# Kernel optimization log

Measured on AMD Instinct MI355X. Metric: run time of the kernel, lower is better.

## Reference

```python
import math
import jax, jax.numpy as jnp
import numpy as np

jax.config.update("jax_enable_x64", True)

P_PRIME = 1000003            # prime modulus; p-1 = 2*3*166667
N_FACTORS = (2, 3, 166667)   # prime factors of p-1 (for primitive-root search)
B, NPATCH, L, K, DIM = 4, 784, 9, 16, 28  # batch, patches/sample, patch len, kernels, map dim


def _modpow(base, exp, p, nbits=21):
    """Vectorized modular exponentiation (square-and-multiply), int64, exponents < 2^nbits."""
    shape = jnp.broadcast_shapes(jnp.shape(base), jnp.shape(exp))
    b0 = jnp.broadcast_to(jnp.asarray(base, jnp.int64) % p, shape)
    e = jnp.broadcast_to(jnp.asarray(exp, jnp.int64), shape)
    def body(i, c):
        res, b = c
        res = jnp.where(((e >> i) & 1) == 1, (res * b) % p, res)
        return (res, (b * b) % p)
    res, _ = jax.lax.fori_loop(0, nbits, body, (jnp.ones(shape, jnp.int64), b0))
    return res


def _decrypt_ips(ct0, cts, y, sk_y, g, p):
    """IPFE decrypt + BSGS discrete log. ct0:[B,P] cts:[B,P,L] y:[K,L] sk_y:[K] -> signed ip [K,B,P]."""
    n = p - 1
    powed = _modpow(cts[None], jnp.mod(y, n)[:, None, None, :], p)   # [K,B,P,L]
    num = powed[..., 0]
    for i in range(1, L):                                            # fixed small L=9
        num = (num * powed[..., i]) % p
    denom = _modpow(ct0[None], jnp.mod(sk_y, n)[:, None, None], p)   # [K,B,P]
    val = (num * _modpow(denom, p - 2, p)) % p                       # = g^{<x,y>} mod p (Fermat inverse)
    # baby-step giant-step over group order n
    m = math.isqrt(n - 1) + 1
    n_giant = -(-n // m)
    baby = _modpow(jnp.int64(g), jnp.arange(m, dtype=jnp.int64), p)  # g^j, j in [0,m)
    order = jnp.argsort(baby)
    sb = baby[order]
    ginv_m = _modpow(jnp.int64(g), jnp.int64((n - m) % n), p)        # g^{-m}
    pt = _modpow(ginv_m, jnp.arange(n_giant, dtype=jnp.int64), p)    # g^{-m*i}
    gamma = (val.reshape(-1)[:, None] * pt[None, :]) % p             # [T, n_giant] giant steps
    pos = jnp.clip(jnp.searchsorted(sb, gamma), 0, m - 1)
    hit = sb[pos] == gamma
    cand = jnp.arange(n_giant, dtype=jnp.int64)[None, :] * m + order[pos]
    ip = jnp.min(jnp.where(hit, cand, n), axis=1)                    # unique match: ip = i*m + j
    ip = jnp.where(ip > n // 2, ip - n, ip)                          # signed representative
    return ip.reshape(K, ct0.shape[0], ct0.shape[1])


def _bn(x, g_, b_, m_, v_):
    s = g_ * jax.lax.rsqrt(v_ + 1e-5)
    return (x - m_[None, :, None, None]) * s[None, :, None, None] + b_[None, :, None, None]


def _conv(x, w, b):
    o = jax.lax.conv_general_dilated(x, w, (1, 1), ((1, 1), (1, 1)),
                                     dimension_numbers=("NCHW", "OIHW", "NCHW"))
    return o + b[None, :, None, None]


def _pool(x):
    return jax.lax.reduce_window(x, jnp.array(-jnp.inf, x.dtype), jax.lax.max,
                                 (1, 1, 2, 2), (1, 1, 2, 2), "VALID")


def _forward(ct0, cts, y, sk_y, bias1, bn1_g, bn1_b, bn1_m, bn1_v,
             conv2_w, conv2_b, bn2_g, bn2_b, bn2_m, bn2_v,
             conv3_w, conv3_b, bn3_g, bn3_b, bn3_m, bn3_v,
             fc1_w, fc1_b, fc2_w, fc2_b, g, p):
    ip = _decrypt_ips(ct0, cts, y, sk_y, g, p)                       # [K,B,P] int64
    maps = ip.astype(jnp.float32) / 10000.0 + bias1[:, None, None]   # dequantize + conv1 bias
    feat = jnp.transpose(maps, (1, 0, 2)).reshape(-1, K, DIM, DIM)   # [B,16,28,28]
    feat = _pool(jax.nn.relu(_bn(feat, bn1_g, bn1_b, bn1_m, bn1_v)))
    feat = _pool(jax.nn.relu(_bn(_conv(feat, conv2_w, conv2_b), bn2_g, bn2_b, bn2_m, bn2_v)))
    feat = _pool(jax.nn.relu(_bn(_conv(feat, conv3_w, conv3_b), bn3_g, bn3_b, bn3_m, bn3_v)))
    flat = feat.reshape(feat.shape[0], -1)                           # [B,576]
    h = jax.nn.relu(flat @ fc1_w.T + fc1_b)                          # dropout = identity (eval mode)
    return h @ fc2_w.T + fc2_b                                       # [B,10]


def setup_inputs():
    rng = np.random.default_rng(0)
    p, n = P_PRIME, P_PRIME - 1
    assert all(p % d for d in range(2, math.isqrt(p) + 1))           # p prime
    g = next(gg for gg in range(2, 200)
             if all(pow(gg, n // q, p) != 1 for q in N_FACTORS))      # primitive root mod p
    s = rng.integers(1, n, size=L)                                    # master secret
    pk = [pow(g, int(si), p) for si in s]
    y = rng.integers(-50, 51, size=(K, L)).astype(np.int64)          # round(w*10000)
    x = rng.integers(0, 21, size=(B, NPATCH, L))                     # quantized patch values
    r = rng.integers(1, n, size=(B, NPATCH))
    gx = [pow(g, t, p) for t in range(21)]
    ct0 = np.zeros((B, NPATCH), dtype=np.int64)
    cts = np.zeros((B, NPATCH, L), dtype=np.int64)
    for b in range(B):
        for j in range(NPATCH):
            rr = int(r[b, j])
            ct0[b, j] = pow(g, rr, p)
            for i in range(L):
                cts[b, j, i] = pow(pk[i], rr, p) * gx[x[b, j, i]] % p
    sk_y = np.array([sum(int(s[i]) * int(y[k, i]) for i in range(L)) % n
                     for k in range(K)], dtype=np.int64)
    f32 = lambda a: jnp.asarray(a, jnp.float32)
    def rn(*sh):
        return f32(rng.standard_normal(sh) * 0.1)
    def bnp(c):
        return (f32(1.0 + 0.1 * rng.standard_normal(c)), rn(c), rn(c), f32(rng.random(c) + 0.5))
    bn1_g, bn1_b, bn1_m, bn1_v = bnp(16)
    bn2_g, bn2_b, bn2_m, bn2_v = bnp(32)
    bn3_g, bn3_b, bn3_m, bn3_v = bnp(64)
    return dict(ct0=jnp.asarray(ct0), cts=jnp.asarray(cts),
                y=jnp.asarray(y), sk_y=jnp.asarray(sk_y), bias1=rn(K),
                bn1_g=bn1_g, bn1_b=bn1_b, bn1_m=bn1_m, bn1_v=bn1_v,
                conv2_w=rn(32, 16, 3, 3), conv2_b=rn(32),
                bn2_g=bn2_g, bn2_b=bn2_b, bn2_m=bn2_m, bn2_v=bn2_v,
                conv3_w=rn(64, 32, 3, 3), conv3_b=rn(64),
                bn3_g=bn3_g, bn3_b=bn3_b, bn3_m=bn3_m, bn3_v=bn3_v,
                fc1_w=rn(128, 576), fc1_b=rn(128),
                fc2_w=rn(10, 128), fc2_b=rn(10), g=g, p=p)


def reference(ct0, cts, y, sk_y, bias1, bn1_g, bn1_b, bn1_m, bn1_v,
              conv2_w, conv2_b, bn2_g, bn2_b, bn2_m, bn2_v,
              conv3_w, conv3_b, bn3_g, bn3_b, bn3_m, bn3_v,
              fc1_w, fc1_b, fc2_w, fc2_b, g, p):
    return _forward(ct0, cts, y, sk_y, bias1, bn1_g, bn1_b, bn1_m, bn1_v,
                    conv2_w, conv2_b, bn2_g, bn2_b, bn2_m, bn2_v,
                    conv3_w, conv3_b, bn3_g, bn3_b, bn3_m, bn3_v,
                    fc1_w, fc1_b, fc2_w, fc2_b, g, p)
```

## Files before the change

kernel.cpp:

```cpp
#include <hip/hip_runtime.h>
#include <stdint.h>

#define PRIME 1000003u
#define NORD  1000002u
#define KCH   16
#define BATCH 4
#define NPATCH 784
#define LLEN  9
#define IPMAX 9000
#define TBLN  (2*IPMAX+1)
#define NBLK  128
#define TPB   832

#define CTR_OFF   2000064
#define POOL_OFF  2008256
#define S2G_OFF   2058432
#define S3G_OFF   2083520
#define HG_OFF    2092736

__device__ __forceinline__ uint32_t mmul(uint32_t a, uint32_t b) {
    uint64_t t = (uint64_t)a * (uint64_t)b;
    uint32_t q = (uint32_t)((t * 2199016ull) >> 41);
    uint32_t r = (uint32_t)t - q * PRIME;
    return (r >= PRIME) ? r - PRIME : r;
}

__device__ __forceinline__ uint32_t mpow(uint32_t base, uint32_t exp) {
    uint32_t r = 1u, b = base;
    while (exp) {
        if (exp & 1u) r = mmul(r, b);
        b = mmul(b, b);
        exp >>= 1;
    }
    return r;
}

__device__ __forceinline__ void cstore(float* p, float v) {
    __hip_atomic_store(p, v, __ATOMIC_RELAXED, __HIP_MEMORY_SCOPE_AGENT);
}
__device__ __forceinline__ float cload(const float* p) {
    return __hip_atomic_load(p, __ATOMIC_RELAXED, __HIP_MEMORY_SCOPE_AGENT);
}

__device__ __forceinline__ void arrive32(unsigned* ctrs, int bid) {
    __syncthreads();
    if (threadIdx.x == 0)
        __hip_atomic_fetch_add(&ctrs[(bid & 31) * 16], 1u,
                               __ATOMIC_RELAXED, __HIP_MEMORY_SCOPE_AGENT);
}
__device__ __forceinline__ void wait32(unsigned* ctrs, unsigned target) {
    if (threadIdx.x == 0) {
        for (;;) {
            unsigned s = 0;
#pragma unroll
            for (int i = 0; i < 32; i++)
                s += __hip_atomic_load(&ctrs[i * 16],
                                       __ATOMIC_RELAXED, __HIP_MEMORY_SCOPE_AGENT);
            if (s >= target) break;
            __builtin_amdgcn_s_sleep(8);
        }
    }
    __syncthreads();
}

__global__ void build_table(const int* __restrict__ g_in, int16_t* __restrict__ table,
                            unsigned* __restrict__ ctrs) {
    int e = blockIdx.x * blockDim.x + threadIdx.x;
    if (e >= TBLN) return;
    if (e < 32)
        __hip_atomic_store(&ctrs[e * 16], 0u, __ATOMIC_RELAXED, __HIP_MEMORY_SCOPE_AGENT);
    int es = e - IPMAX;
    uint32_t exp = (es >= 0) ? (uint32_t)es : (uint32_t)(es + (int)NORD);
    table[mpow((uint32_t)g_in[0], exp)] = (int16_t)es;
}

__global__ void __launch_bounds__(TPB) fused(
    const int* __restrict__ ct0, const int* __restrict__ cts,
    const int* __restrict__ y, const int* __restrict__ sk_y,
    const float* __restrict__ bias1,
    const float* __restrict__ bn1_g, const float* __restrict__ bn1_b,
    const float* __restrict__ bn1_m, const float* __restrict__ bn1_v,
    const float* __restrict__ conv2_w, const float* __restrict__ conv2_b,
    const float* __restrict__ bn2_g, const float* __restrict__ bn2_b,
    const float* __restrict__ bn2_m, const float* __restrict__ bn2_v,
    const float* __restrict__ conv3_w, const float* __restrict__ conv3_b,
    const float* __restrict__ bn3_g, const float* __restrict__ bn3_b,
    const float* __restrict__ bn3_m, const float* __restrict__ bn3_v,
    const float* __restrict__ fc1_w, const float* __restrict__ fc1_b,
    const float* __restrict__ fc2_w, const float* __restrict__ fc2_b,
    const int16_t* __restrict__ table,
    float* __restrict__ pooled, float* __restrict__ s2g, float* __restrict__ s3g,
    float* __restrict__ hg, float* __restrict__ out, unsigned* __restrict__ ctrs) {

    __shared__ union {
        float raw[392];
        struct { float s1p[16][16][16]; float w[4][144]; float co[4][196]; } c2;
        struct { float s2p[32][9][9];  float w[4][288]; float co[4][49]; } c3;
        struct { float s3[576]; float w[8 * 576]; } d1;
        struct { float h[128]; float w[10 * 128]; } d2;
    } sm;

    const int bid = blockIdx.x;
    const int tid = threadIdx.x;

    {
        const int pair = bid >> 1, half = bid & 1;
        const int k = pair & 15, b = pair >> 4;
        const int* yrow = y + k * LLEN;
        int yv[LLEN];
#pragma unroll
        for (int i = 0; i < LLEN; i++) yv[i] = yrow[i];
        const uint32_t sk = (uint32_t)sk_y[k];
        const float sc  = bn1_g[k] * rsqrtf(bn1_v[k] + 1e-5f);
        const float shf = (bias1[k] - bn1_m[k]) * sc + bn1_b[k];

        if (tid < 392) {
            const int j = half * 392 + tid;
            const int* crow = cts + ((b * NPATCH) + j) * LLEN;
            uint32_t c[LLEN];
#pragma unroll
            for (int i = 0; i < LLEN; i++) c[i] = (uint32_t)crow[i];

            uint32_t accp = 1u, accn = 1u;
#pragma unroll
            for (int bit = 5; bit >= 0; bit--) {
                accp = mmul(accp, accp);
                accn = mmul(accn, accn);
#pragma unroll
                for (int i = 0; i < LLEN; i++) {
                    int yi = yv[i];
                    int ay = (yi > 0) ? yi : -yi;
                    if ((ay >> bit) & 1) {
                        if (yi > 0) accp = mmul(accp, c[i]);
                        else        accn = mmul(accn, c[i]);
                    }
                }
            }

            uint32_t den = mmul(mpow((uint32_t)ct0[b * NPATCH + j], sk), accn);
            uint32_t val = mmul(accp, mpow(den, PRIME - 2u));

            int ip = (int)table[val];
            sm.raw[tid] = fmaxf(fmaf((float)ip, sc * 1e-4f, shf), 0.0f);
        }
        __syncthreads();
        if (tid < 98) {
            int pyl = tid / 14, px = tid % 14;
            const float* r0 = &sm.raw[(2 * pyl) * 28 + 2 * px];
            float m = fmaxf(fmaxf(r0[0], r0[1]), fmaxf(r0[28], r0[29]));
            cstore(&pooled[((b * KCH) + k) * 196 + (half * 7 + pyl) * 14 + px], m);
        }
    }
    arrive32(ctrs, bid);
    if (bid >= 64) return;

    if (bid < 32) {
        const int b = bid >> 3, base_oc = (bid & 7) * 4;

        for (int i = tid; i < 16 * 16 * 16; i += TPB)
            ((float*)sm.c2.s1p)[i] = 0.0f;
        if (tid < 576) sm.c2.w[tid / 144][tid % 144] =
            conv2_w[(base_oc + tid / 144) * 144 + tid % 144];

        wait32(ctrs, 128);

        for (int i = tid; i < 16 * 196; i += TPB) {
            int ic = i / 196, pos = i % 196;
            sm.c2.s1p[ic][pos / 14 + 1][pos % 14 + 1] =
                cload(&pooled[((b * KCH) + ic) * 196 + pos]);
        }
        __syncthreads();

        if (tid < 784) {
            int ocs = tid / 196, pos = tid % 196;
            int oh = pos / 14, ow = pos % 14;
            int oc = base_oc + ocs;
            float a0 = 0.0f, a1 = 0.0f, a2 = 0.0f;
#pragma unroll
            for (int ic = 0; ic < 16; ic++) {
                const float* wp = &sm.c2.w[ocs][ic * 9];
                const float* sp = &sm.c2.s1p[ic][oh][ow];
                a0 = fmaf(sp[0],  wp[0], fmaf(sp[1],  wp[1], fmaf(sp[2],  wp[2], a0)));
                a1 = fmaf(sp[16], wp[3], fmaf(sp[17], wp[4], fmaf(sp[18], wp[5], a1)));
                a2 = fmaf(sp[32], wp[6], fmaf(sp[33], wp[7], fmaf(sp[34], wp[8], a2)));
            }
            float sc = bn2_g[oc] * rsqrtf(bn2_v[oc] + 1e-5f);
            float shf = bn2_b[oc] - bn2_m[oc] * sc;
            sm.c2.co[ocs][pos] = fmaxf((a0 + a1 + a2 + conv2_b[oc]) * sc + shf, 0.0f);
        }
        __syncthreads();

        if (tid < 196) {
            int ocs = tid / 49, pp = tid % 49;
            int oh = pp / 7, ow = pp % 7;
            const float* c0 = &sm.c2.co[ocs][(2 * oh) * 14 + 2 * ow];
            cstore(&s2g[((b * 32 + base_oc + ocs) * 49) + pp],
                   fmaxf(fmaxf(c0[0], c0[1]), fmaxf(c0[14], c0[15])));
        }
        arrive32(ctrs, bid);
    }

    {
        const int b = bid >> 4, ocg = bid & 15;

        for (int i = tid; i < 32 * 81; i += TPB)
            ((float*)sm.c3.s2p)[i] = 0.0f;
        for (int i = tid; i < 4 * 288; i += TPB) {
            int w2 = i / 288, rr = i % 288;
            sm.c3.w[w2][rr] = conv3_w[(ocg * 4 + w2) * 288 + rr];
        }

        wait32(ctrs, 160);

        for (int i = tid; i < 32 * 49; i += TPB) {
            int ic = i / 49, pos = i % 49;
            sm.c3.s2p[ic][pos / 7 + 1][pos % 7 + 1] =
                cload(&s2g[((b * 32 + ic) * 49) + pos]);
        }
        __syncthreads();

        const int wid = tid >> 6, lane = tid & 63;
        if (wid < 4 && lane < 49) {
            int oh = lane / 7, ow = lane % 7;
            float a0 = 0.0f, a1 = 0.0f, a2 = 0.0f;
#pragma unroll
            for (int ic = 0; ic < 32; ic++) {
                const float* wp = &sm.c3.w[wid][ic * 9];
                const float* sp = &sm.c3.s2p[ic][oh][ow];
                a0 = fmaf(sp[0],  wp[0], fmaf(sp[1],  wp[1], fmaf(sp[2],  wp[2], a0)));
                a1 = fmaf(sp[9],  wp[3], fmaf(sp[10], wp[4], fmaf(sp[11], wp[5], a1)));
                a2 = fmaf(sp[18], wp[6], fmaf(sp[19], wp[7], fmaf(sp[20], wp[8], a2)));
            }
            int oc = ocg * 4 + wid;
            float sc = bn3_g[oc] * rsqrtf(bn3_v[oc] + 1e-5f);
            float shf = bn3_b[oc] - bn3_m[oc] * sc;
            sm.c3.co[wid][lane] = fmaxf((a0 + a1 + a2 + conv3_b[oc]) * sc + shf, 0.0f);
        }
        __syncthreads();

        if (tid < 36) {
            int w2 = tid / 9, p = tid % 9;
            int oh = p / 3, ow = p % 3;
            const float* c0 = &sm.c3.co[w2][(2 * oh) * 7 + 2 * ow];
            cstore(&s3g[b * 576 + (ocg * 4 + w2) * 9 + p],
                   fmaxf(fmaxf(c0[0], c0[1]), fmaxf(c0[7], c0[8])));
        }
        arrive32(ctrs, bid);
    }

    {
        const int b = bid >> 4, og = bid & 15;

        for (int i = tid; i < 8 * 576; i += TPB)
            sm.d1.w[i] = fc1_w[og * 8 * 576 + i];

        wait32(ctrs, 224);

        if (tid < 576) sm.d1.s3[tid] = cload(&s3g[b * 576 + tid]);
        __syncthreads();

        const int wid = tid >> 6, lane = tid & 63;
        if (wid < 8) {
            int o = og * 8 + wid;
            const float* w = sm.d1.w + wid * 576;
            float acc = 0.0f;
#pragma unroll
            for (int jj = 0; jj < 9; jj++)
                acc = fmaf(sm.d1.s3[jj * 64 + lane], w[jj * 64 + lane], acc);
#pragma unroll
            for (int off = 32; off; off >>= 1) acc += __shfl_down(acc, off);
            if (lane == 0) cstore(&hg[b * 128 + o], fmaxf(acc + fc1_b[o], 0.0f));
        }
        arrive32(ctrs, bid);
    }
    if (bid >= BATCH) return;

    {
        const int b = bid;
        for (int i = tid; i < 10 * 128; i += TPB) sm.d2.w[i] = fc2_w[i];

        wait32(ctrs, 288);

        if (tid < 128) sm.d2.h[tid] = cload(&hg[b * 128 + tid]);
        __syncthreads();

        const int wid = tid >> 6, lane = tid & 63;
        if (wid < 10) {
            const float* w = sm.d2.w + wid * 128;
            float acc = fmaf(sm.d2.h[lane], w[lane], 0.0f);
            acc = fmaf(sm.d2.h[64 + lane], w[64 + lane], acc);
#pragma unroll
            for (int off = 32; off; off >>= 1) acc += __shfl_down(acc, off);
            if (lane == 0) out[b * 10 + wid] = acc + fc2_b[wid];
        }
    }
}

extern "C" void kernel_launch(void* const* d_in, const int* in_sizes, int n_in,
                              void* d_out, int out_size, void* d_ws, size_t ws_size,
                              hipStream_t stream) {
    const int*   ct0    = (const int*)d_in[0];
    const int*   cts    = (const int*)d_in[1];
    const int*   y      = (const int*)d_in[2];
    const int*   sk_y   = (const int*)d_in[3];
    const float* bias1  = (const float*)d_in[4];
    const float* bn1_g  = (const float*)d_in[5];
    const float* bn1_b  = (const float*)d_in[6];
    const float* bn1_m  = (const float*)d_in[7];
    const float* bn1_v  = (const float*)d_in[8];
    const float* conv2_w = (const float*)d_in[9];
    const float* conv2_b = (const float*)d_in[10];
    const float* bn2_g  = (const float*)d_in[11];
    const float* bn2_b  = (const float*)d_in[12];
    const float* bn2_m  = (const float*)d_in[13];
    const float* bn2_v  = (const float*)d_in[14];
    const float* conv3_w = (const float*)d_in[15];
    const float* conv3_b = (const float*)d_in[16];
    const float* bn3_g  = (const float*)d_in[17];
    const float* bn3_b  = (const float*)d_in[18];
    const float* bn3_m  = (const float*)d_in[19];
    const float* bn3_v  = (const float*)d_in[20];
    const float* fc1_w  = (const float*)d_in[21];
    const float* fc1_b  = (const float*)d_in[22];
    const float* fc2_w  = (const float*)d_in[23];
    const float* fc2_b  = (const float*)d_in[24];
    const int*   g_in   = (const int*)d_in[25];
    float* out = (float*)d_out;

    char* ws = (char*)d_ws;
    int16_t*  table = (int16_t*)ws;
    unsigned* ctrs  = (unsigned*)(ws + CTR_OFF);
    float* pooled = (float*)(ws + POOL_OFF);
    float* s2g    = (float*)(ws + S2G_OFF);
    float* s3g    = (float*)(ws + S3G_OFF);
    float* hg     = (float*)(ws + HG_OFF);

    build_table<<<(TBLN + 255) / 256, 256, 0, stream>>>(g_in, table, ctrs);

    fused<<<NBLK, TPB, 0, stream>>>(
        ct0, cts, y, sk_y, bias1, bn1_g, bn1_b, bn1_m, bn1_v,
        conv2_w, conv2_b, bn2_g, bn2_b, bn2_m, bn2_v,
        conv3_w, conv3_b, bn3_g, bn3_b, bn3_m, bn3_v,
        fc1_w, fc1_b, fc2_w, fc2_b, table, pooled, s2g, s3g, hg, out, ctrs);
}
```

Baseline: 135.4 us.

## Fuse conv3 partial sums into conv2 blocks via atomics; fold fc layers

Each conv2 block now computes its 4-channel slice of conv3 as partial sums and accumulates them into a global buffer with atomicAdd. This removes the separate conv3 stage and one grid-wide barrier. The fc1 and fc2 layers are merged into one stage that adds fc2 partials atomically into a zeroed output, removing two more barriers. Block size rises to 1024 and the spin-wait sleep is shortened. In exchange the code relies on float atomics, so summation order is nondeterministic, and conv3 work is now concentrated in 32 blocks.

```diff
diff --git a/kernel.cpp b/kernel.cpp
--- a/kernel.cpp
+++ b/kernel.cpp
@@ -10,13 +10,11 @@
 #define IPMAX 9000
 #define TBLN  (2*IPMAX+1)
 #define NBLK  128
-#define TPB   832
+#define TPB   1024
 
 #define CTR_OFF   2000064
 #define POOL_OFF  2008256
-#define S2G_OFF   2058432
-#define S3G_OFF   2083520
-#define HG_OFF    2092736
+#define C3P_OFF   2058432
 
 __device__ __forceinline__ uint32_t mmul(uint32_t a, uint32_t b) {
     uint64_t t = (uint64_t)a * (uint64_t)b;
@@ -57,18 +55,21 @@
                 s += __hip_atomic_load(&ctrs[i * 16],
                                        __ATOMIC_RELAXED, __HIP_MEMORY_SCOPE_AGENT);
             if (s >= target) break;
-            __builtin_amdgcn_s_sleep(8);
+            __builtin_amdgcn_s_sleep(4);
         }
     }
     __syncthreads();
 }
 
 __global__ void build_table(const int* __restrict__ g_in, int16_t* __restrict__ table,
-                            unsigned* __restrict__ ctrs) {
+                            unsigned* __restrict__ ctrs, float* __restrict__ c3pre,
+                            float* __restrict__ out) {
     int e = blockIdx.x * blockDim.x + threadIdx.x;
     if (e >= TBLN) return;
     if (e < 32)
         __hip_atomic_store(&ctrs[e * 16], 0u, __ATOMIC_RELAXED, __HIP_MEMORY_SCOPE_AGENT);
+    if (e < BATCH * 64 * 49) cstore(&c3pre[e], 0.0f);
+    if (e < BATCH * 10) cstore(&out[e], 0.0f);
     int es = e - IPMAX;
     uint32_t exp = (es >= 0) ? (uint32_t)es : (uint32_t)(es + (int)NORD);
     table[mpow((uint32_t)g_in[0], exp)] = (int16_t)es;
@@ -89,15 +90,23 @@
     const float* __restrict__ fc1_w, const float* __restrict__ fc1_b,
     const float* __restrict__ fc2_w, const float* __restrict__ fc2_b,
     const int16_t* __restrict__ table,
-    float* __restrict__ pooled, float* __restrict__ s2g, float* __restrict__ s3g,
-    float* __restrict__ hg, float* __restrict__ out, unsigned* __restrict__ ctrs) {
+    float* __restrict__ pooled, float* __restrict__ c3pre,
+    float* __restrict__ out, unsigned* __restrict__ ctrs) {
 
     __shared__ union {
         float raw[392];
-        struct { float s1p[16][16][16]; float w[4][144]; float co[4][196]; } c2;
-        struct { float s2p[32][9][9];  float w[4][288]; float co[4][49]; } c3;
-        struct { float s3[576]; float w[8 * 576]; } d1;
-        struct { float h[128]; float w[10 * 128]; } d2;
+        struct {
+            float s1p[16][16][16];
+            float w2[4][144];
+            float co[4][196];
+            float s2p[4][9][9];
+            float w3s[64 * 36];
+        } b;
+        struct {
+            float w[16 * 576];
+            float s3[576];
+            float h[16];
+        } cd;
     } sm;
 
     const int bid = blockIdx.x;
@@ -152,21 +161,26 @@
         }
     }
     arrive32(ctrs, bid);
-    if (bid >= 64) return;
 
     if (bid < 32) {
         const int b = bid >> 3, base_oc = (bid & 7) * 4;
 
         for (int i = tid; i < 16 * 16 * 16; i += TPB)
-            ((float*)sm.c2.s1p)[i] = 0.0f;
-        if (tid < 576) sm.c2.w[tid / 144][tid % 144] =
+            ((float*)sm.b.s1p)[i] = 0.0f;
+        for (int i = tid; i < 4 * 81; i += TPB)
+            ((float*)sm.b.s2p)[i] = 0.0f;
+        if (tid < 576) sm.b.w2[tid / 144][tid % 144] =
             conv2_w[(base_oc + tid / 144) * 144 + tid % 144];
+        for (int i = tid; i < 64 * 36; i += TPB) {
+            int oc = i / 36, j = (i % 36) / 9, t = i % 9;
+            sm.b.w3s[i] = conv3_w[(oc * 32 + base_oc + j) * 9 + t];
+        }
 
         wait32(ctrs, 128);
 
         for (int i = tid; i < 16 * 196; i += TPB) {
             int ic = i / 196, pos = i % 196;
-            sm.c2.s1p[ic][pos / 14 + 1][pos % 14 + 1] =
+            sm.b.s1p[ic][pos / 14 + 1][pos % 14 + 1] =
                 cload(&pooled[((b * KCH) + ic) * 196 + pos]);
         }
         __syncthreads();
@@ -178,120 +192,94 @@
             float a0 = 0.0f, a1 = 0.0f, a2 = 0.0f;
 #pragma unroll
             for (int ic = 0; ic < 16; ic++) {
-                const float* wp = &sm.c2.w[ocs][ic * 9];
-                const float* sp = &sm.c2.s1p[ic][oh][ow];
+                const float* wp = &sm.b.w2[ocs][ic * 9];
+                const float* sp = &sm.b.s1p[ic][oh][ow];
                 a0 = fmaf(sp[0],  wp[0], fmaf(sp[1],  wp[1], fmaf(sp[2],  wp[2], a0)));
                 a1 = fmaf(sp[16], wp[3], fmaf(sp[17], wp[4], fmaf(sp[18], wp[5], a1)));
                 a2 = fmaf(sp[32], wp[6], fmaf(sp[33], wp[7], fmaf(sp[34], wp[8], a2)));
             }
             float sc = bn2_g[oc] * rsqrtf(bn2_v[oc] + 1e-5f);
             float shf = bn2_b[oc] - bn2_m[oc] * sc;
-            sm.c2.co[ocs][pos] = fmaxf((a0 + a1 + a2 + conv2_b[oc]) * sc + shf, 0.0f);
+            sm.b.co[ocs][pos] = fmaxf((a0 + a1 + a2 + conv2_b[oc]) * sc + shf, 0.0f);
         }
         __syncthreads();
 
         if (tid < 196) {
             int ocs = tid / 49, pp = tid % 49;
             int oh = pp / 7, ow = pp % 7;
-            const float* c0 = &sm.c2.co[ocs][(2 * oh) * 14 + 2 * ow];
-            cstore(&s2g[((b * 32 + base_oc + ocs) * 49) + pp],
-                   fmaxf(fmaxf(c0[0], c0[1]), fmaxf(c0[14], c0[15])));
-        }
-        arrive32(ctrs, bid);
-    }
-
-    {
-        const int b = bid >> 4, ocg = bid & 15;
-
-        for (int i = tid; i < 32 * 81; i += TPB)
-            ((float*)sm.c3.s2p)[i] = 0.0f;
-        for (int i = tid; i < 4 * 288; i += TPB) {
-            int w2 = i / 288, rr = i % 288;
-            sm.c3.w[w2][rr] = conv3_w[(ocg * 4 + w2) * 288 + rr];
-        }
-
-        wait32(ctrs, 160);
-
-        for (int i = tid; i < 32 * 49; i += TPB) {
-            int ic = i / 49, pos = i % 49;
-            sm.c3.s2p[ic][pos / 7 + 1][pos % 7 + 1] =
-                cload(&s2g[((b * 32 + ic) * 49) + pos]);
-        }
-        __syncthreads();
-
-        const int wid = tid >> 6, lane = tid & 63;
-        if (wid < 4 && lane < 49) {
-            int oh = lane / 7, ow = lane % 7;
+            const float* c0 = &sm.b.co[ocs][(2 * oh) * 14 + 2 * ow];
+            sm.b.s2p[ocs][oh + 1][ow + 1] =
+                fmaxf(fmaxf(c0[0], c0[1]), fmaxf(c0[14], c0[15]));
+        }
+        __syncthreads();
+
+        for (int i = tid; i < 64 * 49; i += TPB) {
+            int oc = i / 49, pos = i % 49;
+            int oh = pos / 7, ow = pos % 7;
             float a0 = 0.0f, a1 = 0.0f, a2 = 0.0f;
 #pragma unroll
-            for (int ic = 0; ic < 32; ic++) {
-                const float* wp = &sm.c3.w[wid][ic * 9];
-                const float* sp = &sm.c3.s2p[ic][oh][ow];
+            for (int j = 0; j < 4; j++) {
+                const float* wp = &sm.b.w3s[oc * 36 + j * 9];
+                const float* sp = &sm.b.s2p[j][oh][ow];
                 a0 = fmaf(sp[0],  wp[0], fmaf(sp[1],  wp[1], fmaf(sp[2],  wp[2], a0)));
                 a1 = fmaf(sp[9],  wp[3], fmaf(sp[10], wp[4], fmaf(sp[11], wp[5], a1)));
                 a2 = fmaf(sp[18], wp[6], fmaf(sp[19], wp[7], fmaf(sp[20], wp[8], a2)));
             }
-            int oc = ocg * 4 + wid;
+            atomicAdd(&c3pre[(b * 64 + oc) * 49 + pos], a0 + a1 + a2);
+        }
+        arrive32(ctrs, bid);
+        return;
+    }
+    if (bid >= 64) return;
+
+    {
+        const int bb = bid - 32;
+        const int b = bb >> 3, og = bb & 7;
+
+        {
+            const float4* src = (const float4*)(fc1_w + og * 16 * 576);
+            float4* dst = (float4*)sm.cd.w;
+            for (int i = tid; i < 16 * 576 / 4; i += TPB) dst[i] = src[i];
+        }
+
+        wait32(ctrs, 160);
+
+        if (tid < 576) {
+            int oc = tid / 9, p = tid % 9;
+            int oh = p / 3, ow = p % 3;
+            const float* base = &c3pre[(b * 64 + oc) * 49];
+            int idx = (2 * oh) * 7 + 2 * ow;
             float sc = bn3_g[oc] * rsqrtf(bn3_v[oc] + 1e-5f);
             float shf = bn3_b[oc] - bn3_m[oc] * sc;
-            sm.c3.co[wid][lane] = fmaxf((a0 + a1 + a2 + conv3_b[oc]) * sc + shf, 0.0f);
-        }
-        __syncthreads();
-
-        if (tid < 36) {
-            int w2 = tid / 9, p = tid % 9;
-            int oh = p / 3, ow = p % 3;
-            const float* c0 = &sm.c3.co[w2][(2 * oh) * 7 + 2 * ow];
-            cstore(&s3g[b * 576 + (ocg * 4 + w2) * 9 + p],
-                   fmaxf(fmaxf(c0[0], c0[1]), fmaxf(c0[7], c0[8])));
-        }
-        arrive32(ctrs, bid);
-    }
-
-    {
-        const int b = bid >> 4, og = bid & 15;
-
-        for (int i = tid; i < 8 * 576; i += TPB)
-            sm.d1.w[i] = fc1_w[og * 8 * 576 + i];
-
-        wait32(ctrs, 224);
-
-        if (tid < 576) sm.d1.s3[tid] = cload(&s3g[b * 576 + tid]);
+            float cb = conv3_b[oc];
+            float r0 = fmaxf((cload(base + idx)     + cb) * sc + shf, 0.0f);
+            float r1 = fmaxf((cload(base + idx + 1) + cb) * sc + shf, 0.0f);
+            float r2 = fmaxf((cload(base + idx + 7) + cb) * sc + shf, 0.0f);
+            float r3 = fmaxf((cload(base + idx + 8) + cb) * sc + shf, 0.0f);
+            sm.cd.s3[tid] = fmaxf(fmaxf(r0, r1), fmaxf(r2, r3));
+        }
         __syncthreads();
 
         const int wid = tid >> 6, lane = tid & 63;
-        if (wid < 8) {
-            int o = og * 8 + wid;
-            const float* w = sm.d1.w + wid * 576;
+        {
+            int o = og * 16 + wid;
+            const float* w = sm.cd.w + wid * 576;
             float acc = 0.0f;
 #pragma unroll
             for (int jj = 0; jj < 9; jj++)
-                acc = fmaf(sm.d1.s3[jj * 64 + lane], w[jj * 64 + lane], acc);
+                acc = fmaf(sm.cd.s3[jj * 64 + lane], w[jj * 64 + lane], acc);
 #pragma unroll
             for (int off = 32; off; off >>= 1) acc += __shfl_down(acc, off);
-            if (lane == 0) cstore(&hg[b * 128 + o], fmaxf(acc + fc1_b[o], 0.0f));
-        }
-        arrive32(ctrs, bid);
-    }
-    if (bid >= BATCH) return;
-
-    {
-        const int b = bid;
-        for (int i = tid; i < 10 * 128; i += TPB) sm.d2.w[i] = fc2_w[i];
-
-        wait32(ctrs, 288);
-
-        if (tid < 128) sm.d2.h[tid] = cload(&hg[b * 128 + tid]);
-        __syncthreads();
-
-        const int wid = tid >> 6, lane = tid & 63;
-        if (wid < 10) {
-            const float* w = sm.d2.w + wid * 128;
-            float acc = fmaf(sm.d2.h[lane], w[lane], 0.0f);
-            acc = fmaf(sm.d2.h[64 + lane], w[64 + lane], acc);
-#pragma unroll
-            for (int off = 32; off; off >>= 1) acc += __shfl_down(acc, off);
-            if (lane == 0) out[b * 10 + wid] = acc + fc2_b[wid];
+            if (lane == 0) sm.cd.h[wid] = fmaxf(acc + fc1_b[o], 0.0f);
+        }
+        __syncthreads();
+
+        if (tid < 10) {
+            float acc = (og == 0) ? fc2_b[tid] : 0.0f;
+            const float* w = fc2_w + tid * 128 + og * 16;
+#pragma unroll
+            for (int j = 0; j < 16; j++) acc = fmaf(sm.cd.h[j], w[j], acc);
+            atomicAdd(&out[b * 10 + tid], acc);
         }
     }
 }
@@ -331,15 +319,13 @@
     int16_t*  table = (int16_t*)ws;
     unsigned* ctrs  = (unsigned*)(ws + CTR_OFF);
     float* pooled = (float*)(ws + POOL_OFF);
-    float* s2g    = (float*)(ws + S2G_OFF);
-    float* s3g    = (float*)(ws + S3G_OFF);
-    float* hg     = (float*)(ws + HG_OFF);
-
-    build_table<<<(TBLN + 255) / 256, 256, 0, stream>>>(g_in, table, ctrs);
+    float* c3pre  = (float*)(ws + C3P_OFF);
+
+    build_table<<<(TBLN + 255) / 256, 256, 0, stream>>>(g_in, table, ctrs, c3pre, out);
 
     fused<<<NBLK, TPB, 0, stream>>>(
         ct0, cts, y, sk_y, bias1, bn1_g, bn1_b, bn1_m, bn1_v,
         conv2_w, conv2_b, bn2_g, bn2_b, bn2_m, bn2_v,
         conv3_w, conv3_b, bn3_g, bn3_b, bn3_m, bn3_v,
-        fc1_w, fc1_b, fc2_w, fc2_b, table, pooled, s2g, s3g, hg, out, ctrs);
-}
+        fc1_w, fc1_b, fc2_w, fc2_b, table, pooled, c3pre, out, ctrs);
+}
```

Measured after the change: 132.4 us. 2.2% less time.
